# Kernel tuning notes

Measured on AMD Instinct MI355X. Metric: run time of the kernel, lower is better.

## Reference

```python
import jax, jax.numpy as jnp
import numpy as np

L, B, D_IN, H = 1024, 64, 512, 512


def setup_inputs() -> dict:
    key = jax.random.key(0)
    ks = jax.random.split(key, 9)
    s = 1.0 / np.sqrt(H)
    inp = {
        "inputs": jax.random.normal(ks[0], (L, B, D_IN), dtype=jnp.float32),
        # canonical chain tree: node at step t is node t (left child = t-1)
        "indexes": jnp.broadcast_to(jnp.arange(L, dtype=jnp.int32)[:, None], (L, B)),
        # gate linears: ih has bias, lhh/rhh do not (per nn.Linear defs)
        "W_gih": jax.random.uniform(ks[1], (5 * H, D_IN), jnp.float32, -s, s),
        "b_gih": jax.random.uniform(ks[2], (5 * H,), jnp.float32, -s, s),
        "W_glhh": jax.random.uniform(ks[3], (5 * H, H), jnp.float32, -s, s),
        "W_grhh": jax.random.uniform(ks[4], (5 * H, H), jnp.float32, -s, s),
        "W_cih": jax.random.uniform(ks[5], (H, D_IN), jnp.float32, -s, s),
        "b_cih": jax.random.uniform(ks[6], (H,), jnp.float32, -s, s),
        "W_clhh": jax.random.uniform(ks[7], (H, H), jnp.float32, -s, s),
        "W_crhh": jax.random.uniform(ks[8], (H, H), jnp.float32, -s, s),
    }
    return inp


def _tree_gru(inputs, W_gih, b_gih, W_glhh, W_grhh, W_cih, b_cih, W_clhh, W_crhh):
    # chain tree: left_child_h = previous hidden, right_child_h = 0 (leaf side)
    batch = inputs.shape[1]
    hidden = W_clhh.shape[0]
    h0 = jnp.zeros((batch, hidden), inputs.dtype)

    def step(h_prev, x_t):
        left = h_prev
        right = jnp.zeros_like(h_prev)
        gates = jax.nn.sigmoid(
            x_t @ W_gih.T + b_gih + left @ W_glhh.T + right @ W_grhh.T
        )
        rl, rr, zl, zr, z = jnp.split(gates, 5, axis=1)
        cell = jnp.tanh(
            x_t @ W_cih.T + b_cih + (rl * left) @ W_clhh.T + (rr * right) @ W_crhh.T
        )
        h = zl * left + zr * right + z * cell  # node_forward hidden
        return h, h

    _, hs = jax.lax.scan(step, h0, inputs)  # hs: [L, B, H]
    outputs = jnp.transpose(hs, (1, 0, 2))  # [B, L, H], batch-first like original
    output_t = jnp.zeros((batch, hidden), inputs.dtype)  # original returns zeros
    return outputs, output_t


def reference(inputs, indexes, W_gih, b_gih, W_glhh, W_grhh, W_cih, b_cih,
              W_clhh, W_crhh):
    del indexes  # chain ordering: indexes[step, b] == step
    return _tree_gru(inputs, W_gih, b_gih, W_glhh, W_grhh,
                     W_cih, b_cih, W_clhh, W_crhh)
```

## Files before the change

### kernel.cpp

```cpp
#include <hip/hip_runtime.h>
#include <hip/hip_bf16.h>
#include <stdint.h>

typedef __bf16 bf16;
typedef __bf16 bf16x8 __attribute__((ext_vector_type(8)));
typedef __bf16 bf16x4 __attribute__((ext_vector_type(4)));
typedef float f32x16 __attribute__((ext_vector_type(16)));
typedef float f32x4 __attribute__((ext_vector_type(4)));

#define LL 1024
#define BB 64
#define HH 512
#define NR 8
#define NC 16
#define NWG (NR + NC)
#define NPROD 32
#define NLAUNCH (NWG + NPROD)
#define WSLOT 16
#define MFMA32(a, b, c) __builtin_amdgcn_mfma_f32_32x32x16_bf16(a, b, c, 0, 0, 0)

#define OFF_X      ((size_t)0)
#define OFF_WGSEL  ((size_t)67108864)
#define OFF_WCIH   ((size_t)68681728)
#define OFF_WHHZZ  ((size_t)69206016)
#define OFF_HBUF   ((size_t)70254592)
#define OFF_A2     ((size_t)70385664)
#define OFF_CTR    ((size_t)70516736)
#define OFF_XS     ((size_t)70517760)

static __device__ __forceinline__ float sigm(float x) {
  return 1.0f / (1.0f + __expf(-x));
}
static __device__ __forceinline__ float tanhx(float x) {
  x = fminf(15.0f, fmaxf(-15.0f, x));
  float e = __expf(2.0f * x);
  return (e - 1.0f) / (e + 1.0f);
}

static __device__ __forceinline__ unsigned ld_stamp(const unsigned* p) {
  unsigned s;
  asm volatile("global_load_dword %0, %1, off sc0 sc1\n\ts_waitcnt vmcnt(0)"
               : "=v"(s) : "v"(p) : "memory");
  return s;
}
static __device__ __forceinline__ void st_stamp(unsigned* p, unsigned v) {
  asm volatile("global_store_dword %0, %1, off sc0 sc1" :: "v"(p), "v"(v) : "memory");
}
static __device__ __forceinline__ void ld_frag(const bf16* p, bf16x8& d) {
  asm volatile("global_load_dwordx4 %0, %1, off sc0 sc1" : "=v"(d) : "v"(p) : "memory");
}
static __device__ __forceinline__ void ld_frag_c(const bf16* p, bf16x8& d) {
  asm volatile("global_load_dwordx4 %0, %1, off" : "=v"(d) : "v"(p) : "memory");
}
static __device__ __forceinline__ void ld_f4(const float* p, f32x4& d) {
  asm volatile("global_load_dwordx4 %0, %1, off sc0 sc1" : "=v"(d) : "v"(p) : "memory");
}
static __device__ __forceinline__ void st_f4(float* p, f32x4 v) {
  asm volatile("global_store_dwordx4 %0, %1, off sc0 sc1" :: "v"(p), "v"(v) : "memory");
}
static __device__ __forceinline__ void st_u16(bf16* p, unsigned v) {
  asm volatile("global_store_short %0, %1, off sc0 sc1" :: "v"(p), "v"(v) : "memory");
}
#define VWAIT(n) do { asm volatile("s_waitcnt vmcnt(" #n ")" ::: "memory"); \
                      __builtin_amdgcn_sched_barrier(0); } while (0)

static __device__ __forceinline__ bf16x8 ldsfrag(const bf16* w, int i, int k) {
  unsigned byte = ((unsigned)i << 10) + ((unsigned)k << 1);
  byte ^= ((unsigned)(i & 7) << 4);
  return *(const bf16x8*)((const char*)w + byte);
}

__global__ __launch_bounds__(256) void k_cvt_x(const float* __restrict__ in,
                                               bf16* __restrict__ o) {
  size_t i = ((size_t)blockIdx.x * 256 + threadIdx.x) * 4;
  float4 f = *(const float4*)(in + i);
  bf16x4 v;
  v[0] = (bf16)f.x; v[1] = (bf16)f.y; v[2] = (bf16)f.z; v[3] = (bf16)f.w;
  *(bf16x4*)(o + i) = v;
}

__global__ __launch_bounds__(256) void k_cvt_w(const float* __restrict__ wgih,
                                               const float* __restrict__ wcf,
                                               const float* __restrict__ wglhh,
                                               bf16* __restrict__ wgsel,
                                               bf16* __restrict__ wcb,
                                               bf16* __restrict__ whhzz) {
  int i = blockIdx.x * 256 + threadIdx.x;
  const int NQ1 = (1536 * 512) / 4;
  const int NQ2 = (512 * 512) / 4;
  const float* s;
  bf16* d;
  if (i < NQ1) {
    int e = i * 4;
    int p = e >> 9, k = e & 511;
    int src = (p < 512) ? p : ((p < 1024) ? (1024 + p - 512) : (2048 + p - 1024));
    s = wgih + (size_t)src * 512 + k;
    d = wgsel + (size_t)p * 512 + k;
  } else if (i < NQ1 + NQ2) {
    int e = (i - NQ1) * 4;
    int n = e >> 9, k = e & 511;
    s = wcf + (size_t)n * 512 + k;
    d = wcb + (size_t)n * 512 + k;
  } else {
    int e = (i - NQ1 - NQ2) * 4;
    int q = e >> 9, k = e & 511;
    int src = (q < 512) ? (1024 + q) : (2048 + q - 512);
    s = wglhh + (size_t)src * 512 + k;
    d = whhzz + (size_t)q * 512 + k;
  }
  float4 f = *(const float4*)s;
  bf16x4 v;
  v[0] = (bf16)f.x; v[1] = (bf16)f.y; v[2] = (bf16)f.z; v[3] = (bf16)f.w;
  *(bf16x4*)d = v;
}

__global__ __launch_bounds__(256) void k_main(
    const bf16* __restrict__ xbf, const bf16* __restrict__ wgsel,
    const bf16* __restrict__ wcb, const bf16* __restrict__ whhzz,
    const float* __restrict__ wglhh, const float* __restrict__ wclhh,
    const float* __restrict__ bg, const float* __restrict__ bc,
    float* __restrict__ out, bf16* __restrict__ hbuf,
    bf16* __restrict__ a2buf, float* __restrict__ xs,
    unsigned* __restrict__ ctrs) {
  __shared__ __align__(16) char smem[128 * 1024];
  bf16* wlds = (bf16*)smem;

  const int wg = blockIdx.x, tid = threadIdx.x;
  const int lane = tid & 63, wave = tid >> 6;
  const int lr = lane & 31, kq = (lane >> 5) * 8;
  unsigned* astamp = ctrs;
  unsigned* hstamp = ctrs + 16;
  unsigned* xstamp = ctrs + 64;

  if (wg >= NWG) {
    const int gx = (wg - NWG) * 4 + wave;
    const int proj = gx >> 5;
    const int m0 = 32 * ((gx >> 4) & 1);
    const int col = (gx & 15) * 32 + lr;
    float bias;
    const bf16* wb;
    if (proj == 0)      { bias = bg[col];        wb = wgsel + (size_t)col * HH; }
    else if (proj == 1) { bias = bg[1024 + col]; wb = wgsel + (size_t)(512 + col) * HH; }
    else if (proj == 2) { bias = bg[2048 + col]; wb = wgsel + (size_t)(1024 + col) * HH; }
    else                { bias = bc[col];        wb = wcb + (size_t)col * HH; }
    wb += kq;
    float* xsl = xs + ((size_t)gx * 64 + lane) * 16;
    for (int t = 0; t < LL; ++t) {
      if (t >= WSLOT) {
        const unsigned* sp = hstamp + (lane & 15);
        while (__any((int)(ld_stamp(sp) < (unsigned)(t - WSLOT + 1)))) {}
      }
      f32x16 a;
      #pragma unroll
      for (int r = 0; r < 16; ++r) a[r] = bias;
      const bf16* xa = xbf + (size_t)t * (BB * HH) + (size_t)(m0 + lr) * HH + kq;
      #pragma unroll 4
      for (int kk = 0; kk < 32; ++kk)
        a = MFMA32(*(const bf16x8*)(xa + kk * 16), *(const bf16x8*)(wb + kk * 16), a);
      float* dst = xsl + (size_t)(t & (WSLOT - 1)) * (128 * 64 * 16);
      f32x4 v0, v1, v2, v3;
      #pragma unroll
      for (int e = 0; e < 4; ++e) { v0[e] = a[e]; v1[e] = a[4 + e]; v2[e] = a[8 + e]; v3[e] = a[12 + e]; }
      st_f4(dst, v0); st_f4(dst + 4, v1); st_f4(dst + 8, v2); st_f4(dst + 12, v3);
      asm volatile("s_waitcnt vmcnt(0)" ::: "memory");
      if (lane == 0) st_stamp(xstamp + gx, (unsigned)(t + 1));
    }
    return;
  }
  __builtin_amdgcn_s_setprio(1);

  if (wg < NR) {
    bf16* hstage = (bf16*)(smem + 65536);
    const int m0 = 32 * (wave & 1);
    const int lc = 32 * (wave >> 1) + lr;
    const int p = wg * 64 + lc;
    const int mrow = m0 + 4 * (lane >> 5);
    const int gx = (wave & 1) * 16 + 2 * wg + (wave >> 1);

    for (int u = tid; u < 64 * 64; u += 256) {
      int i = u >> 6, k8 = (u & 63) << 3;
      const float* s = wglhh + (size_t)(wg * 64 + i) * HH + k8;
      bf16x8 v;
      #pragma unroll
      for (int j = 0; j < 8; ++j) v[j] = (bf16)s[j];
      unsigned byte = ((unsigned)i << 10) + ((unsigned)k8 << 1);
      byte ^= ((unsigned)(i & 7) << 4);
      *(bf16x8*)((char*)wlds + byte) = v;
    }
    __syncthreads();

    for (int t = 1; t < LL; ++t) {
      {
        const unsigned* sp = hstamp + (lane & 15);
        unsigned tgt = (unsigned)t;
        if (lane == 16) { sp = xstamp + gx; tgt = (unsigned)(t + 1); }
        while (__any((int)(ld_stamp(sp) < tgt))) {}
      }
      __builtin_amdgcn_sched_barrier(0);
      const float* xsp = xs + (((size_t)(t & (WSLOT - 1)) * 128 + gx) * 64 + lane) * 16;
      f32x4 xv0, xv1, xv2, xv3;
      ld_f4(xsp, xv0); ld_f4(xsp + 4, xv1); ld_f4(xsp + 8, xv2); ld_f4(xsp + 12, xv3);
      const bf16* hs = hbuf + (size_t)((t - 1) & 1) * (BB * HH);
      #pragma unroll
      for (int rnd = 0; rnd < 2; ++rnd) {
        bf16x8 tmp[8];
        #pragma unroll
        for (int j = 0; j < 8; ++j) {
          int u = rnd * 2048 + j * 256 + tid;
          ld_frag(hs + (size_t)(u >> 6) * 512 + ((u & 63) << 3), tmp[j]);
        }
        VWAIT(0);
        #pragma unroll
        for (int j = 0; j < 8; ++j) {
          int u = rnd * 2048 + j * 256 + tid;
          unsigned byte = ((unsigned)(u >> 6) << 10) + ((unsigned)((u & 63) << 3) << 1);
          byte ^= ((unsigned)((u >> 6) & 7) << 4);
          *(bf16x8*)((char*)hstage + byte) = tmp[j];
        }
      }
      __syncthreads();
      f32x16 acc;
      #pragma unroll
      for (int r = 0; r < 16; ++r) acc[r] = 0.0f;
      #pragma unroll 8
      for (int kk = 0; kk < 32; ++kk)
        acc = MFMA32(ldsfrag(hstage, m0 + lr, kk * 16 + kq),
                     ldsfrag(wlds, lc, kk * 16 + kq), acc);
      bf16* ad = a2buf + (size_t)(t & 1) * (BB * HH);
      #pragma unroll
      for (int r = 0; r < 16; ++r) {
        int m = mrow + (r & 3) + 8 * (r >> 2);
        unsigned hb_ = ((unsigned)m << 10) + ((unsigned)p << 1);
        hb_ ^= ((unsigned)(m & 7) << 4);
        float hp = (float)*(const bf16*)((const char*)hstage + hb_);
        float xadd = (r < 4) ? xv0[r & 3] : (r < 8) ? xv1[r & 3]
                   : (r < 12) ? xv2[r & 3] : xv3[r & 3];
        float gg = sigm(acc[r] + xadd);
        bf16 av = (bf16)(gg * hp);
        st_u16(ad + (size_t)m * HH + p, (unsigned)__builtin_bit_cast(unsigned short, av));
      }
      asm volatile("s_waitcnt vmcnt(0)" ::: "memory");
      __syncthreads();
      if (tid == 0) st_stamp(astamp + wg, (unsigned)(t + 1));
    }
  } else {
    const int cj = wg - NR;
    float* zlzs = (float*)(smem + 32768);
    const int n = cj * 32 + lr;
    const bool crit = (wave < 2);
    const int m0 = crit ? 32 * wave : 32 * (wave - 2);
    const int mrow = m0 + 4 * (lane >> 5);
    const int Mq = (m0 >> 5) * 16;
    const int gc = 96 + Mq + cj;
    const int gzl = 32 + Mq + cj;
    const int gz = 64 + Mq + cj;

    for (int u = tid; u < 32 * 64; u += 256) {
      int i = u >> 6, k8 = (u & 63) << 3;
      const float* s = wclhh + (size_t)(cj * 32 + i) * HH + k8;
      bf16x8 v;
      #pragma unroll
      for (int j = 0; j < 8; ++j) v[j] = (bf16)s[j];
      unsigned byte = ((unsigned)i << 10) + ((unsigned)k8 << 1);
      byte ^= ((unsigned)(i & 7) << 4);
      *(bf16x8*)((char*)wlds + byte) = v;
    }
    __syncthreads();

    float hreg[16];
    #pragma unroll
    for (int r = 0; r < 16; ++r) hreg[r] = 0.0f;

    for (int t = 0; t < LL; ++t) {
      if (crit) {
        f32x16 acc;
        #pragma unroll
        for (int r = 0; r < 16; ++r) acc[r] = 0.0f;
        f32x4 xv0, xv1, xv2, xv3;
        if (t > 0) {
          {
            const unsigned* sp = astamp + (lane & 7);
            unsigned tgt = (unsigned)(t + 1);
            if (lane == 8) sp = xstamp + gc;
            while (__any((int)(ld_stamp(sp) < tgt))) {}
          }
          __builtin_amdgcn_sched_barrier(0);
          const float* xsp = xs + (((size_t)(t & (WSLOT - 1)) * 128 + gc) * 64 + lane) * 16;
          ld_f4(xsp, xv0); ld_f4(xsp + 4, xv1); ld_f4(xsp + 8, xv2); ld_f4(xsp + 12, xv3);
          bf16* myst = (bf16*)(smem + 49152 + wave * 32768);
          const bf16* ab = a2buf + (size_t)(t & 1) * (BB * HH) + (size_t)m0 * HH;
          #pragma unroll
          for (int rnd = 0; rnd < 4; ++rnd) {
            bf16x8 tmp[8];
            #pragma unroll
            for (int j = 0; j < 8; ++j) {
              int u = rnd * 512 + j * 64 + lane;
              ld_frag(ab + (size_t)(u >> 6) * 512 + ((u & 63) << 3), tmp[j]);
            }
            VWAIT(0);
            #pragma unroll
            for (int j = 0; j < 8; ++j) {
              int u = rnd * 512 + j * 64 + lane;
              unsigned byte = ((unsigned)(u >> 6) << 10) + ((unsigned)((u & 63) << 3) << 1);
              byte ^= ((unsigned)((u >> 6) & 7) << 4);
              *(bf16x8*)((char*)myst + byte) = tmp[j];
            }
          }
          asm volatile("s_waitcnt lgkmcnt(0)" ::: "memory");
          __builtin_amdgcn_sched_barrier(0);
          #pragma unroll 8
          for (int kk = 0; kk < 32; ++kk)
            acc = MFMA32(ldsfrag(myst, lr, kk * 16 + kq),
                         ldsfrag(wlds, lr, kk * 16 + kq), acc);
        } else {
          {
            const unsigned* sp = xstamp + gc;
            while (__any((int)(ld_stamp(sp) < 1u))) {}
          }
          __builtin_amdgcn_sched_barrier(0);
          const float* xsp = xs + ((size_t)gc * 64 + lane) * 16;
          ld_f4(xsp, xv0); ld_f4(xsp + 4, xv1); ld_f4(xsp + 8, xv2); ld_f4(xsp + 12, xv3);
          VWAIT(0);
        }
        #pragma unroll
        for (int r = 0; r < 16; ++r) {
          float xadd = (r < 4) ? xv0[r & 3] : (r < 8) ? xv1[r & 3]
                     : (r < 12) ? xv2[r & 3] : xv3[r & 3];
          acc[r] += xadd;
        }
        __syncthreads();
        bf16* hd = hbuf + (size_t)(t & 1) * (BB * HH);
        #pragma unroll
        for (int r = 0; r < 16; ++r) {
          int m = mrow + (r & 3) + 8 * (r >> 2);
          float zlv = zlzs[m * 32 + lr];
          float zv = zlzs[2048 + m * 32 + lr];
          float h = zlv * hreg[r] + zv * tanhx(acc[r]);
          hreg[r] = h;
          bf16 hb16 = (bf16)h;
          st_u16(hd + (size_t)m * HH + n, (unsigned)__builtin_bit_cast(unsigned short, hb16));
        }
        asm volatile("s_waitcnt vmcnt(0)" ::: "memory");
      } else {
        f32x16 azl, az;
        #pragma unroll
        for (int r = 0; r < 16; ++r) { azl[r] = 0.0f; az[r] = 0.0f; }
        f32x4 l0, l1, l2, l3, z0, z1, z2, z3;
        if (t > 0) {
          {
            const unsigned* sp = hstamp + (lane & 15);
            unsigned tgt = (unsigned)t;
            if (lane == 16) { sp = xstamp + gzl; tgt = (unsigned)(t + 1); }
            if (lane == 17) { sp = xstamp + gz; tgt = (unsigned)(t + 1); }
            while (__any((int)(ld_stamp(sp) < tgt))) {}
          }
          __builtin_amdgcn_sched_barrier(0);
          const float* xl = xs + (((size_t)(t & (WSLOT - 1)) * 128 + gzl) * 64 + lane) * 16;
          const float* xz = xs + (((size_t)(t & (WSLOT - 1)) * 128 + gz) * 64 + lane) * 16;
          ld_f4(xl, l0); ld_f4(xl + 4, l1); ld_f4(xl + 8, l2); ld_f4(xl + 12, l3);
          ld_f4(xz, z0); ld_f4(xz + 4, z1); ld_f4(xz + 8, z2); ld_f4(xz + 12, z3);
          const bf16* hsA = hbuf + (size_t)((t - 1) & 1) * (BB * HH) + (size_t)(m0 + lr) * HH + kq;
          const bf16* bl = whhzz + (size_t)n * HH + kq;
          const bf16* bz = whhzz + (size_t)(512 + n) * HH + kq;
          bf16x8 A[2][4], Wl[2][4], Wz[2][4];
          #pragma unroll
          for (int j = 0; j < 4; ++j) {
            ld_frag(hsA + j * 16, A[0][j]);
            ld_frag_c(bl + j * 16, Wl[0][j]);
            ld_frag_c(bz + j * 16, Wz[0][j]);
          }
          #pragma unroll
          for (int b = 0; b < 8; ++b) {
            const int s = b & 1, ns = s ^ 1;
            if (b < 7) {
              #pragma unroll
              for (int j = 0; j < 4; ++j) {
                ld_frag(hsA + ((b + 1) * 4 + j) * 16, A[ns][j]);
                ld_frag_c(bl + ((b + 1) * 4 + j) * 16, Wl[ns][j]);
                ld_frag_c(bz + ((b + 1) * 4 + j) * 16, Wz[ns][j]);
              }
              VWAIT(12);
            } else {
              VWAIT(0);
            }
            #pragma unroll
            for (int j = 0; j < 4; ++j) {
              azl = MFMA32(A[s][j], Wl[s][j], azl);
              az = MFMA32(A[s][j], Wz[s][j], az);
            }
          }
        } else {
          {
            const unsigned* sp = xstamp + ((lane & 1) ? gz : gzl);
            while (__any((int)(ld_stamp(sp) < 1u))) {}
          }
          __builtin_amdgcn_sched_barrier(0);
          const float* xl = xs + ((size_t)gzl * 64 + lane) * 16;
          const float* xz = xs + ((size_t)gz * 64 + lane) * 16;
          ld_f4(xl, l0); ld_f4(xl + 4, l1); ld_f4(xl + 8, l2); ld_f4(xl + 12, l3);
          ld_f4(xz, z0); ld_f4(xz + 4, z1); ld_f4(xz + 8, z2); ld_f4(xz + 12, z3);
          VWAIT(0);
        }
        #pragma unroll
        for (int r = 0; r < 16; ++r) {
          int m = mrow + (r & 3) + 8 * (r >> 2);
          float xla = (r < 4) ? l0[r & 3] : (r < 8) ? l1[r & 3]
                    : (r < 12) ? l2[r & 3] : l3[r & 3];
          float xza = (r < 4) ? z0[r & 3] : (r < 8) ? z1[r & 3]
                    : (r < 12) ? z2[r & 3] : z3[r & 3];
          zlzs[m * 32 + lr] = sigm(azl[r] + xla);
          zlzs[2048 + m * 32 + lr] = sigm(az[r] + xza);
        }
        __syncthreads();
      }
      __syncthreads();
      if (tid == 0) st_stamp(hstamp + cj, (unsigned)(t + 1));
      if (crit) {
        #pragma unroll
        for (int r = 0; r < 16; ++r) {
          int m = mrow + (r & 3) + 8 * (r >> 2);
          out[(size_t)m * (LL * HH) + (size_t)t * HH + n] = hreg[r];
        }
      }
    }
  }
}

extern "C" void kernel_launch(void* const* d_in, const int* in_sizes, int n_in,
                              void* d_out, int out_size, void* d_ws, size_t ws_size,
                              hipStream_t stream) {
  (void)in_sizes; (void)n_in; (void)out_size; (void)ws_size;
  const float* x     = (const float*)d_in[0];
  const float* wgih  = (const float*)d_in[2];
  const float* bg    = (const float*)d_in[3];
  const float* wglhh = (const float*)d_in[4];
  const float* wcihf = (const float*)d_in[6];
  const float* bc    = (const float*)d_in[7];
  const float* wclhh = (const float*)d_in[8];
  float* out = (float*)d_out;

  char* ws = (char*)d_ws;
  bf16* xbf     = (bf16*)(ws + OFF_X);
  bf16* wgsel   = (bf16*)(ws + OFF_WGSEL);
  bf16* wcb     = (bf16*)(ws + OFF_WCIH);
  bf16* whhzz   = (bf16*)(ws + OFF_WHHZZ);
  bf16* hbuf    = (bf16*)(ws + OFF_HBUF);
  bf16* a2buf   = (bf16*)(ws + OFF_A2);
  float* xsb    = (float*)(ws + OFF_XS);
  unsigned* ctr = (unsigned*)(ws + OFF_CTR);

  hipMemsetAsync(ctr, 0, 1024, stream);
  hipMemsetAsync(out + (size_t)BB * LL * HH, 0, (size_t)BB * HH * sizeof(float), stream);

  k_cvt_x<<<dim3(32768), dim3(256), 0, stream>>>(x, xbf);
  k_cvt_w<<<dim3(1536), dim3(256), 0, stream>>>(wgih, wcihf, wglhh, wgsel, wcb, whhzz);
  k_main<<<dim3(NLAUNCH), dim3(256), 0, stream>>>(xbf, wgsel, wcb, whhzz, wglhh, wclhh,
                                                  bg, bc, out, hbuf, a2buf, xsb, ctr);
}
```

Measured before the change: 12.80 ms.

## Stage a2 activations cooperatively across all four waves into shared LDS

Until now each of the two critical waves in the cell workgroups copied its own 32-row slice of the r*h activation buffer into a private LDS region over four serial rounds. Now all four waves (critical and z-gate waves) each load a quarter of the full 64x512 tile into one shared LDS buffer. A barrier follows, and the critical waves run their MFMA from it. The reset-gate workgroups also issue all 16 fragment loads before a single wait, replacing two rounds. The aim is to spread global-to-LDS traffic over more waves and raise memory-level parallelism on the recurrent critical path, at the cost of higher register pressure and an extra block-wide barrier per step.

```diff
diff --git a/kernel.cpp b/kernel.cpp
--- a/kernel.cpp
+++ b/kernel.cpp
@@ -201,22 +201,19 @@
       f32x4 xv0, xv1, xv2, xv3;
       ld_f4(xsp, xv0); ld_f4(xsp + 4, xv1); ld_f4(xsp + 8, xv2); ld_f4(xsp + 12, xv3);
       const bf16* hs = hbuf + (size_t)((t - 1) & 1) * (BB * HH);
-      #pragma unroll
-      for (int rnd = 0; rnd < 2; ++rnd) {
-        bf16x8 tmp[8];
-        #pragma unroll
-        for (int j = 0; j < 8; ++j) {
-          int u = rnd * 2048 + j * 256 + tid;
-          ld_frag(hs + (size_t)(u >> 6) * 512 + ((u & 63) << 3), tmp[j]);
-        }
-        VWAIT(0);
-        #pragma unroll
-        for (int j = 0; j < 8; ++j) {
-          int u = rnd * 2048 + j * 256 + tid;
-          unsigned byte = ((unsigned)(u >> 6) << 10) + ((unsigned)((u & 63) << 3) << 1);
-          byte ^= ((unsigned)((u >> 6) & 7) << 4);
-          *(bf16x8*)((char*)hstage + byte) = tmp[j];
-        }
+      bf16x8 tmp[16];
+      #pragma unroll
+      for (int j = 0; j < 16; ++j) {
+        int u = j * 256 + tid;
+        ld_frag(hs + (size_t)(u >> 6) * 512 + ((u & 63) << 3), tmp[j]);
+      }
+      VWAIT(0);
+      #pragma unroll
+      for (int j = 0; j < 16; ++j) {
+        int u = j * 256 + tid;
+        unsigned byte = ((unsigned)(u >> 6) << 10) + ((unsigned)((u & 63) << 3) << 1);
+        byte ^= ((unsigned)((u >> 6) & 7) << 4);
+        *(bf16x8*)((char*)hstage + byte) = tmp[j];
       }
       __syncthreads();
       f32x16 acc;
@@ -245,7 +242,8 @@
     }
   } else {
     const int cj = wg - NR;
-    float* zlzs = (float*)(smem + 32768);
+    bf16* a2st = (bf16*)(smem + 32768);
+    float* zlzs = (float*)(smem + 98304);
     const int n = cj * 32 + lr;
     const bool crit = (wave < 2);
     const int m0 = crit ? 32 * wave : 32 * (wave - 2);
@@ -273,9 +271,6 @@
 
     for (int t = 0; t < LL; ++t) {
       if (crit) {
-        f32x16 acc;
-        #pragma unroll
-        for (int r = 0; r < 16; ++r) acc[r] = 0.0f;
         f32x4 xv0, xv1, xv2, xv3;
         if (t > 0) {
           {
@@ -287,31 +282,21 @@
           __builtin_amdgcn_sched_barrier(0);
           const float* xsp = xs + (((size_t)(t & (WSLOT - 1)) * 128 + gc) * 64 + lane) * 16;
           ld_f4(xsp, xv0); ld_f4(xsp + 4, xv1); ld_f4(xsp + 8, xv2); ld_f4(xsp + 12, xv3);
-          bf16* myst = (bf16*)(smem + 49152 + wave * 32768);
-          const bf16* ab = a2buf + (size_t)(t & 1) * (BB * HH) + (size_t)m0 * HH;
-          #pragma unroll
-          for (int rnd = 0; rnd < 4; ++rnd) {
-            bf16x8 tmp[8];
-            #pragma unroll
-            for (int j = 0; j < 8; ++j) {
-              int u = rnd * 512 + j * 64 + lane;
-              ld_frag(ab + (size_t)(u >> 6) * 512 + ((u & 63) << 3), tmp[j]);
-            }
-            VWAIT(0);
-            #pragma unroll
-            for (int j = 0; j < 8; ++j) {
-              int u = rnd * 512 + j * 64 + lane;
-              unsigned byte = ((unsigned)(u >> 6) << 10) + ((unsigned)((u & 63) << 3) << 1);
-              byte ^= ((unsigned)((u >> 6) & 7) << 4);
-              *(bf16x8*)((char*)myst + byte) = tmp[j];
-            }
-          }
-          asm volatile("s_waitcnt lgkmcnt(0)" ::: "memory");
-          __builtin_amdgcn_sched_barrier(0);
-          #pragma unroll 8
-          for (int kk = 0; kk < 32; ++kk)
-            acc = MFMA32(ldsfrag(myst, lr, kk * 16 + kq),
-                         ldsfrag(wlds, lr, kk * 16 + kq), acc);
+          const bf16* ab = a2buf + (size_t)(t & 1) * (BB * HH);
+          bf16x8 tmp[16];
+          #pragma unroll
+          for (int j = 0; j < 16; ++j) {
+            int u = j * 256 + tid;
+            ld_frag(ab + (size_t)(u >> 6) * 512 + ((u & 63) << 3), tmp[j]);
+          }
+          VWAIT(0);
+          #pragma unroll
+          for (int j = 0; j < 16; ++j) {
+            int u = j * 256 + tid;
+            unsigned byte = ((unsigned)(u >> 6) << 10) + ((unsigned)((u & 63) << 3) << 1);
+            byte ^= ((unsigned)((u >> 6) & 7) << 4);
+            *(bf16x8*)((char*)a2st + byte) = tmp[j];
+          }
         } else {
           {
             const unsigned* sp = xstamp + gc;
@@ -322,13 +307,22 @@
           ld_f4(xsp, xv0); ld_f4(xsp + 4, xv1); ld_f4(xsp + 8, xv2); ld_f4(xsp + 12, xv3);
           VWAIT(0);
         }
+        __syncthreads();
+        f32x16 acc;
+        #pragma unroll
+        for (int r = 0; r < 16; ++r) acc[r] = 0.0f;
+        if (t > 0) {
+          #pragma unroll 8
+          for (int kk = 0; kk < 32; ++kk)
+            acc = MFMA32(ldsfrag(a2st, m0 + lr, kk * 16 + kq),
+                         ldsfrag(wlds, lr, kk * 16 + kq), acc);
+        }
         #pragma unroll
         for (int r = 0; r < 16; ++r) {
           float xadd = (r < 4) ? xv0[r & 3] : (r < 8) ? xv1[r & 3]
                      : (r < 12) ? xv2[r & 3] : xv3[r & 3];
           acc[r] += xadd;
         }
-        __syncthreads();
         bf16* hd = hbuf + (size_t)(t & 1) * (BB * HH);
         #pragma unroll
         for (int r = 0; r < 16; ++r) {
@@ -411,6 +405,28 @@
           zlzs[m * 32 + lr] = sigm(azl[r] + xla);
           zlzs[2048 + m * 32 + lr] = sigm(az[r] + xza);
         }
+        if (t > 0) {
+          {
+            const unsigned* sp = astamp + (lane & 7);
+            while (__any((int)(ld_stamp(sp) < (unsigned)(t + 1)))) {}
+          }
+          __builtin_amdgcn_sched_barrier(0);
+          const bf16* ab = a2buf + (size_t)(t & 1) * (BB * HH);
+          bf16x8 tmp[16];
+          #pragma unroll
+          for (int j = 0; j < 16; ++j) {
+            int u = j * 256 + tid;
+            ld_frag(ab + (size_t)(u >> 6) * 512 + ((u & 63) << 3), tmp[j]);
+          }
+          VWAIT(0);
+          #pragma unroll
+          for (int j = 0; j < 16; ++j) {
+            int u = j * 256 + tid;
+            unsigned byte = ((unsigned)(u >> 6) << 10) + ((unsigned)((u & 63) << 3) << 1);
+            byte ^= ((unsigned)((u >> 6) & 7) << 4);
+            *(bf16x8*)((char*)a2st + byte) = tmp[j];
+          }
+        }
         __syncthreads();
       }
       __syncthreads();
```

Result: slower. 13.86 ms (+8.3%).
